# Kernel optimization log

Measured on AMD Instinct MI355X. Metric: run time of the kernel, lower is better.

The kernel has to match this reference:

```python
import jax, jax.numpy as jnp
import numpy as np

N_NODES = 50000


def _segment_mean(vals, seg_ids, num_segments):
    s = jax.ops.segment_sum(vals, seg_ids, num_segments=num_segments)
    cnt = jax.ops.segment_sum(jnp.ones((vals.shape[0],), vals.dtype), seg_ids,
                              num_segments=num_segments)
    return s / jnp.clip(cnt, 1.0)[:, None]


def _sage_layer(h, src, dst, W_self, W_neigh, b):
    # mean-aggregate neighbor messages: gather h[src], scatter-mean to dst
    neigh = _segment_mean(h[src], dst, N_NODES)
    return h @ W_self + neigh @ W_neigh + b


def _edge_score(h, src, dst, Wp, bp):
    # concat(h_u, h_v) @ Wp == h_u @ Wp[:d] + h_v @ Wp[d:]
    d = h.shape[1]
    return h[src] @ Wp[:d] + h[dst] @ Wp[d:] + bp


def setup_inputs() -> dict:
    key = jax.random.key(0)
    ks = jax.random.split(key, 16)
    N, E, EP, EN = N_NODES, 800000, 200000, 200000
    d_in, d_hid, d_out = 128, 256, 128
    inp = {
        'x': jax.random.normal(ks[0], (N, d_in), jnp.float32),
        'msg_src': jax.random.randint(ks[1], (E,), 0, N, jnp.int32),
        'msg_dst': jax.random.randint(ks[2], (E,), 0, N, jnp.int32),
        'pos_src': jax.random.randint(ks[3], (EP,), 0, N, jnp.int32),
        'pos_dst': jax.random.randint(ks[4], (EP,), 0, N, jnp.int32),
        'neg_src': jax.random.randint(ks[5], (EN,), 0, N, jnp.int32),
        'neg_dst': jax.random.randint(ks[6], (EN,), 0, N, jnp.int32),
        'W1_self': jax.random.normal(ks[7], (d_in, d_hid), jnp.float32) * 0.05,
        'W1_neigh': jax.random.normal(ks[8], (d_in, d_hid), jnp.float32) * 0.05,
        'b1': jnp.zeros((d_hid,), jnp.float32),
        'W2_self': jax.random.normal(ks[9], (d_hid, d_out), jnp.float32) * 0.05,
        'W2_neigh': jax.random.normal(ks[10], (d_hid, d_out), jnp.float32) * 0.05,
        'b2': jnp.zeros((d_out,), jnp.float32),
        'Wp': jax.random.normal(ks[11], (2 * d_out, 1), jnp.float32) * 0.05,
        'bp': jnp.zeros((1,), jnp.float32),
    }
    return inp


def reference(x, msg_src, msg_dst, pos_src, pos_dst, neg_src, neg_dst,
              W1_self, W1_neigh, b1, W2_self, W2_neigh, b2, Wp, bp):
    h = _sage_layer(x, msg_src, msg_dst, W1_self, W1_neigh, b1)
    h = jax.nn.relu(h)
    h = _sage_layer(h, msg_src, msg_dst, W2_self, W2_neigh, b2)
    pos_score = _edge_score(h, pos_src, pos_dst, Wp, bp)
    neg_score = _edge_score(h, neg_src, neg_dst, Wp, bp)
    return pos_score, neg_score
```

## Files before the change

### kernel.cpp

```cpp
#include <hip/hip_runtime.h>


#define NN 50000
#define EM 800000
#define EPOS 200000
#define ENEG 200000
#define NB 196
#define RPB 4096
#define MTILES 3125
#define GEMM_GRID 512
#define XCONV_BLOCKS 6250

typedef __bf16 bf16;
typedef bf16 bf16x2 __attribute__((ext_vector_type(2)));
typedef bf16 bf16x4 __attribute__((ext_vector_type(4)));
typedef bf16 bf16x8 __attribute__((ext_vector_type(8)));
typedef float floatx4 __attribute__((ext_vector_type(4)));

#define I_CNT  0
#define I_ROW  50176
#define I_BSUM 100608
#define I_BOFF 100864
#define I_CCUR 101120
#define I_CSR  101376
#define B_CREG 3605504
#define B_XB   10005504
#define B_AGG1 22805504
#define B_H1   35605504
#define B_NV   61205504
#define B_WT1  62005504
#define B_WT2  62136576
#define B_P    62267648
#define B_Q    62468352

__global__ __launch_bounds__(256) void count_kernel(const int* __restrict__ dst,
                                                    int* __restrict__ cnt, int n) {
    int i = blockIdx.x * blockDim.x + threadIdx.x;
    if (i < n) atomicAdd(&cnt[dst[i]], 1);
}

__global__ __launch_bounds__(256) void scan1_kernel(const int* __restrict__ cnt,
                                                    int* __restrict__ bsum) {
    __shared__ int s[256];
    int t = threadIdx.x;
    int i = blockIdx.x * 256 + t;
    s[t] = (i < NN) ? cnt[i] : 0;
    __syncthreads();
    for (int o = 128; o > 0; o >>= 1) {
        if (t < o) s[t] += s[t + o];
        __syncthreads();
    }
    if (t == 0) bsum[blockIdx.x] = s[0];
}

__global__ __launch_bounds__(256) void scan2_kernel(const int* __restrict__ bsum,
                                                    int* __restrict__ boff) {
    __shared__ int s[256];
    int t = threadIdx.x;
    s[t] = (t < NB) ? bsum[t] : 0;
    __syncthreads();
    for (int o = 1; o < 256; o <<= 1) {
        int u = (t >= o) ? s[t - o] : 0;
        __syncthreads();
        s[t] += u;
        __syncthreads();
    }
    if (t < NB) boff[t] = (t == 0) ? 0 : s[t - 1];
}

__global__ __launch_bounds__(256) void scan3_kernel(const int* __restrict__ cnt,
                                                    const int* __restrict__ boff,
                                                    int* __restrict__ rowstart,
                                                    int* __restrict__ ccur) {
    __shared__ int s[256];
    int t = threadIdx.x;
    int i = blockIdx.x * 256 + t;
    int v = (i < NN) ? cnt[i] : 0;
    s[t] = v;
    __syncthreads();
    for (int o = 1; o < 256; o <<= 1) {
        int u = (t >= o) ? s[t - o] : 0;
        __syncthreads();
        s[t] += u;
        __syncthreads();
    }
    int excl = boff[blockIdx.x] + s[t] - v;
    if (i < NN) rowstart[i] = excl;
    if (i == NN - 1) rowstart[NN] = EM;
    if (t == 0) ccur[blockIdx.x] = boff[blockIdx.x];
}

__global__ __launch_bounds__(256) void bin_kernel(const int* __restrict__ src,
                                                  const int* __restrict__ dst,
                                                  int* __restrict__ ccur,
                                                  unsigned long long* __restrict__ creg) {
    __shared__ int hist[NB];
    __shared__ int cnt2[NB];
    __shared__ int goff[NB];
    __shared__ int base[256];
    __shared__ unsigned long long sorted[RPB];
    int t = threadIdx.x;
    int e0 = blockIdx.x * RPB;
    int nrec = EM - e0; if (nrec > RPB) nrec = RPB;

    for (int i = t; i < NB; i += 256) { hist[i] = 0; cnt2[i] = 0; }
    __syncthreads();

    int myb[RPB / 256];
    unsigned long long myrec[RPB / 256];
#pragma unroll
    for (int j = 0; j < RPB / 256; ++j) {
        int idx = j * 256 + t;
        if (idx < nrec) {
            int s = src[e0 + idx], d = dst[e0 + idx];
            myb[j] = d >> 8;
            myrec[j] = ((unsigned long long)(unsigned)d << 32) | (unsigned)s;
            atomicAdd(&hist[myb[j]], 1);
        } else myb[j] = -1;
    }
    __syncthreads();

    base[t] = (t < NB) ? hist[t] : 0;
    __syncthreads();
    for (int o = 1; o < 256; o <<= 1) {
        int u = (t >= o) ? base[t - o] : 0;
        __syncthreads();
        base[t] += u;
        __syncthreads();
    }

    if (t < NB && hist[t] > 0) goff[t] = atomicAdd(&ccur[t], hist[t]);
#pragma unroll
    for (int j = 0; j < RPB / 256; ++j) {
        if (myb[j] >= 0) {
            int rk = atomicAdd(&cnt2[myb[j]], 1);
            sorted[base[myb[j]] - hist[myb[j]] + rk] = myrec[j];
        }
    }
    __syncthreads();

#pragma unroll
    for (int j = 0; j < RPB / 256; ++j) {
        int idx = j * 256 + t;
        if (idx < nrec) {
            unsigned long long rec = sorted[idx];
            int b = (int)(rec >> 40);
            int exb = base[b] - hist[b];
            creg[(size_t)goff[b] + (idx - exb)] = rec;
        }
    }
}

__global__ __launch_bounds__(256) void binsort_kernel(
    const unsigned long long* __restrict__ creg,
    const int* __restrict__ rowstart, int* __restrict__ csr) {
    __shared__ int lcur[256];
    int t = threadIdx.x;
    int node0 = blockIdx.x * 256;
    int nodes = NN - node0; if (nodes > 256) nodes = 256;
    if (t < nodes) lcur[t] = rowstart[node0 + t];
    __syncthreads();
    int beg = rowstart[node0];
    int end = rowstart[node0 + nodes];
    for (int i = beg + t; i < end; i += 256) {
        unsigned long long rec = creg[i];
        int s = (int)(rec & 0xffffffffu);
        int d = (int)(rec >> 32);
        int pos = atomicAdd(&lcur[d - node0], 1);
        csr[pos] = s;
    }
}

__global__ __launch_bounds__(256) void conv_kernel(
    const float* __restrict__ x, bf16* __restrict__ xb,
    const float* __restrict__ W1s, const float* __restrict__ W1n,
    const float* __restrict__ W2n, const float* __restrict__ W2s,
    bf16* __restrict__ Wt1, bf16* __restrict__ Wt2) {
    if (blockIdx.x < XCONV_BLOCKS) {
        int i = blockIdx.x * 256 + threadIdx.x;
        float4 v = ((const float4*)x)[i];
        bf16x4 o;
        o[0] = (bf16)v.x; o[1] = (bf16)v.y; o[2] = (bf16)v.z; o[3] = (bf16)v.w;
        *(bf16x4*)(xb + (size_t)i * 4) = o;
    } else {
        int i = (blockIdx.x - XCONV_BLOCKS) * 256 + threadIdx.x;
        if (i >= 65536) return;
        int n = i >> 8, k = i & 255;
        float w1 = (k < 128) ? W1s[k * 256 + n] : W1n[(k - 128) * 256 + n];
        Wt1[i] = (bf16)w1;
        float w2 = (n < 128) ? W2n[k * 128 + n] : W2s[k * 128 + (n - 128)];
        Wt2[i] = (bf16)w2;
    }
}

__global__ __launch_bounds__(256) void gather1_kernel(const bf16* __restrict__ feat,
                                                      const int* __restrict__ rowstart,
                                                      const int* __restrict__ csr,
                                                      bf16* __restrict__ agg) {
    int node = (blockIdx.x * 256 + threadIdx.x) >> 6;
    if (node >= NN) return;
    int lane = threadIdx.x & 63;
    int q = lane >> 4, r = lane & 15;
    int c = r * 8;
    int beg = rowstart[node], end = rowstart[node + 1];
    float acc[8] = {0.f, 0.f, 0.f, 0.f, 0.f, 0.f, 0.f, 0.f};
    for (int i = beg + q; i < end; i += 4) {
        int s = csr[i];
        bf16x8 v = *(const bf16x8*)(feat + (size_t)s * 128 + c);
#pragma unroll
        for (int u = 0; u < 8; ++u) acc[u] += (float)v[u];
    }
#pragma unroll
    for (int m = 16; m <= 32; m <<= 1)
#pragma unroll
        for (int u = 0; u < 8; ++u) acc[u] += __shfl_xor(acc[u], m);
    if (q == 0) {
        int deg = end - beg;
        float inv = 1.0f / (float)(deg > 0 ? deg : 1);
        bf16x8 o;
#pragma unroll
        for (int u = 0; u < 8; ++u) o[u] = (bf16)(acc[u] * inv);
        *(bf16x8*)(agg + (size_t)node * 128 + c) = o;
    }
}

__global__ __launch_bounds__(256) void gemm1_kernel(
    const bf16* __restrict__ xb, const bf16* __restrict__ aggb,
    const bf16* __restrict__ Wt, const float* __restrict__ b1,
    bf16* __restrict__ h1b) {
    int w = threadIdx.x >> 6;
    int lane = threadIdx.x & 63;
    int r = lane & 15, quad = lane >> 4;
    int colbase = w * 64;

    bf16x8 bfr[4][8];
#pragma unroll
    for (int t = 0; t < 4; ++t)
#pragma unroll
        for (int kk = 0; kk < 8; ++kk)
            bfr[t][kk] = *(const bf16x8*)(Wt + (size_t)(colbase + t * 16 + r) * 256
                                          + kk * 32 + quad * 8);
    float bb[4];
#pragma unroll
    for (int t = 0; t < 4; ++t) bb[t] = b1[colbase + t * 16 + r];

    for (int tile = blockIdx.x; tile < MTILES; tile += GEMM_GRID) {
        int m0 = tile * 16;
        int row = m0 + r;
        bf16x8 a[8];
#pragma unroll
        for (int kk = 0; kk < 4; ++kk)
            a[kk] = *(const bf16x8*)(xb + (size_t)row * 128 + kk * 32 + quad * 8);
#pragma unroll
        for (int kk = 4; kk < 8; ++kk)
            a[kk] = *(const bf16x8*)(aggb + (size_t)row * 128 + (kk - 4) * 32 + quad * 8);
        floatx4 acc[4];
#pragma unroll
        for (int t = 0; t < 4; ++t) acc[t] = (floatx4){0.f, 0.f, 0.f, 0.f};
#pragma unroll
        for (int kk = 0; kk < 8; ++kk)
#pragma unroll
            for (int t = 0; t < 4; ++t)
                acc[t] = __builtin_amdgcn_mfma_f32_16x16x32_bf16(a[kk], bfr[t][kk],
                                                                 acc[t], 0, 0, 0);
        int mb = m0 + quad * 4;
#pragma unroll
        for (int t = 0; t < 4; ++t) {
            int col = colbase + t * 16 + r;
#pragma unroll
            for (int rr = 0; rr < 4; ++rr) {
                float v = acc[t][rr] + bb[t];
                v = v > 0.f ? v : 0.f;
                h1b[(size_t)(mb + rr) * 256 + col] = (bf16)v;
            }
        }
    }
}

__global__ __launch_bounds__(256) void gemm2_kernel(
    const bf16* __restrict__ h1b, const bf16* __restrict__ Wt,
    const float* __restrict__ b2, const float* __restrict__ wp,
    float4* __restrict__ nodev) {
    __shared__ float lp[4][16];
    __shared__ float lq[4][16];
    int w = threadIdx.x >> 6;
    int lane = threadIdx.x & 63;
    int r = lane & 15, quad = lane >> 4;
    int colbase = w * 64;

    bf16x8 bfr[4][8];
#pragma unroll
    for (int t = 0; t < 4; ++t)
#pragma unroll
        for (int kk = 0; kk < 8; ++kk)
            bfr[t][kk] = *(const bf16x8*)(Wt + (size_t)(colbase + t * 16 + r) * 256
                                          + kk * 32 + quad * 8);
    float bb[4], wA[4], wB[4];
#pragma unroll
    for (int t = 0; t < 4; ++t) {
        int col = colbase + t * 16 + r;
        if (w < 2) {
            bb[t] = 0.f;
            wA[t] = wp[col];
            wB[t] = wp[128 + col];
        } else {
            int c2 = col - 128;
            bb[t] = b2[c2];
            wA[t] = wp[c2];
            wB[t] = wp[128 + c2];
        }
    }

    for (int tile = blockIdx.x; tile < MTILES; tile += GEMM_GRID) {
        int m0 = tile * 16;
        int row = m0 + r;
        bf16x8 a[8];
#pragma unroll
        for (int kk = 0; kk < 8; ++kk)
            a[kk] = *(const bf16x8*)(h1b + (size_t)row * 256 + kk * 32 + quad * 8);
        floatx4 acc[4];
#pragma unroll
        for (int t = 0; t < 4; ++t) acc[t] = (floatx4){0.f, 0.f, 0.f, 0.f};
#pragma unroll
        for (int kk = 0; kk < 8; ++kk)
#pragma unroll
            for (int t = 0; t < 4; ++t)
                acc[t] = __builtin_amdgcn_mfma_f32_16x16x32_bf16(a[kk], bfr[t][kk],
                                                                 acc[t], 0, 0, 0);
        float pacc[4], qacc[4];
#pragma unroll
        for (int rr = 0; rr < 4; ++rr) {
            float pr = 0.f, qr = 0.f;
#pragma unroll
            for (int t = 0; t < 4; ++t) {
                float v = acc[t][rr] + bb[t];
                pr += v * wA[t];
                qr += v * wB[t];
            }
            pacc[rr] = pr;
            qacc[rr] = qr;
        }
#pragma unroll
        for (int m = 1; m <= 8; m <<= 1) {
#pragma unroll
            for (int rr = 0; rr < 4; ++rr) {
                pacc[rr] += __shfl_xor(pacc[rr], m);
                qacc[rr] += __shfl_xor(qacc[rr], m);
            }
        }
        if (r == 0) {
#pragma unroll
            for (int rr = 0; rr < 4; ++rr) {
                lp[w][quad * 4 + rr] = pacc[rr];
                lq[w][quad * 4 + rr] = qacc[rr];
            }
        }
        __syncthreads();
        if (threadIdx.x < 16) {
            int rw = threadIdx.x;
            float4 o;
            o.x = lp[0][rw] + lp[1][rw];
            o.y = lq[0][rw] + lq[1][rw];
            o.z = lp[2][rw] + lp[3][rw];
            o.w = lq[2][rw] + lq[3][rw];
            nodev[m0 + rw] = o;
        }
        __syncthreads();
    }
}

__global__ __launch_bounds__(256) void gather2_kernel(
    const float4* __restrict__ nodev, const int* __restrict__ rowstart,
    const int* __restrict__ csr, float* __restrict__ p, float* __restrict__ q) {
    int t = threadIdx.x;
    int node = blockIdx.x * 16 + (t >> 4);
    if (node >= NN) return;
    int l = t & 15;
    int beg = rowstart[node], end = rowstart[node + 1];
    float pz = 0.f, qz = 0.f;
    for (int i = beg + l; i < end; i += 16) {
        float4 v = nodev[csr[i]];
        pz += v.x;
        qz += v.y;
    }
#pragma unroll
    for (int m = 8; m >= 1; m >>= 1) {
        pz += __shfl_xor(pz, m);
        qz += __shfl_xor(qz, m);
    }
    if (l == 0) {
        int deg = end - beg;
        float inv = 1.0f / (float)(deg > 0 ? deg : 1);
        float4 me = nodev[node];
        p[node] = me.z + pz * inv;
        q[node] = me.w + qz * inv;
    }
}

__global__ __launch_bounds__(256) void score_kernel(
    const int* __restrict__ psrc, const int* __restrict__ pdst,
    const int* __restrict__ nsrc, const int* __restrict__ ndst,
    const float* __restrict__ p, const float* __restrict__ q,
    const float* __restrict__ bp, float* __restrict__ out) {
    int i = blockIdx.x * blockDim.x + threadIdx.x;
    float b = bp[0];
    if (i < EPOS) {
        out[i] = p[psrc[i]] + q[pdst[i]] + b;
    } else if (i < EPOS + ENEG) {
        int j = i - EPOS;
        out[i] = p[nsrc[j]] + q[ndst[j]] + b;
    }
}

extern "C" void kernel_launch(void* const* d_in, const int* in_sizes, int n_in,
                              void* d_out, int out_size, void* d_ws, size_t ws_size,
                              hipStream_t stream) {
    const float* x    = (const float*)d_in[0];
    const int*   msrc = (const int*)d_in[1];
    const int*   mdst = (const int*)d_in[2];
    const int*   psrc = (const int*)d_in[3];
    const int*   pdst = (const int*)d_in[4];
    const int*   nsrc = (const int*)d_in[5];
    const int*   ndst = (const int*)d_in[6];
    const float* W1s  = (const float*)d_in[7];
    const float* W1n  = (const float*)d_in[8];
    const float* b1   = (const float*)d_in[9];
    const float* W2s  = (const float*)d_in[10];
    const float* W2n  = (const float*)d_in[11];
    const float* b2   = (const float*)d_in[12];
    const float* wp   = (const float*)d_in[13];
    const float* bp   = (const float*)d_in[14];

    char* ws = (char*)d_ws;
    int*   cnt      = (int*)ws + I_CNT;
    int*   rowstart = (int*)ws + I_ROW;
    int*   bsum     = (int*)ws + I_BSUM;
    int*   boff     = (int*)ws + I_BOFF;
    int*   ccur     = (int*)ws + I_CCUR;
    int*   csr_src  = (int*)ws + I_CSR;
    unsigned long long* creg = (unsigned long long*)(ws + B_CREG);
    bf16*   xb    = (bf16*)(ws + B_XB);
    bf16*   agg1b = (bf16*)(ws + B_AGG1);
    bf16*   h1b   = (bf16*)(ws + B_H1);
    float4* nodev = (float4*)(ws + B_NV);
    bf16*   Wt1   = (bf16*)(ws + B_WT1);
    bf16*   Wt2   = (bf16*)(ws + B_WT2);
    float*  p     = (float*)(ws + B_P);
    float*  q     = (float*)(ws + B_Q);
    float*  out   = (float*)d_out;

    hipMemsetAsync(cnt, 0, 50176 * sizeof(int), stream);

    count_kernel<<<(EM + 255) / 256, 256, 0, stream>>>(mdst, cnt, EM);
    scan1_kernel<<<NB, 256, 0, stream>>>(cnt, bsum);
    scan2_kernel<<<1, 256, 0, stream>>>(bsum, boff);
    scan3_kernel<<<NB, 256, 0, stream>>>(cnt, boff, rowstart, ccur);
    bin_kernel<<<(EM + RPB - 1) / RPB, 256, 0, stream>>>(msrc, mdst, ccur, creg);
    binsort_kernel<<<NB, 256, 0, stream>>>(creg, rowstart, csr_src);

    conv_kernel<<<XCONV_BLOCKS + 256, 256, 0, stream>>>(x, xb, W1s, W1n, W2n, W2s,
                                                        Wt1, Wt2);

    gather1_kernel<<<(NN + 3) / 4, 256, 0, stream>>>(xb, rowstart, csr_src, agg1b);
    gemm1_kernel<<<GEMM_GRID, 256, 0, stream>>>(xb, agg1b, Wt1, b1, h1b);
    gemm2_kernel<<<GEMM_GRID, 256, 0, stream>>>(h1b, Wt2, b2, wp, nodev);
    gather2_kernel<<<(NN + 15) / 16, 256, 0, stream>>>(nodev, rowstart, csr_src, p, q);
    score_kernel<<<(EPOS + ENEG + 255) / 256, 256, 0, stream>>>(
        psrc, pdst, nsrc, ndst, p, q, bp, out);
}
```

Before: 263.7 us.

## Fuse CSR count into conversion kernel and fuse layer-1 gather into GEMM

Result: slower. 284.4 us (+7.9%).

```diff
diff --git a/kernel.cpp b/kernel.cpp
--- a/kernel.cpp
+++ b/kernel.cpp
@@ -7,227 +7,185 @@
 #define ENEG 200000
 #define NB 196
 #define RPB 4096
+#define CBLK 196
 #define MTILES 3125
 #define GEMM_GRID 512
 #define XCONV_BLOCKS 6250
 
 typedef __bf16 bf16;
-typedef bf16 bf16x2 __attribute__((ext_vector_type(2)));
 typedef bf16 bf16x4 __attribute__((ext_vector_type(4)));
 typedef bf16 bf16x8 __attribute__((ext_vector_type(8)));
 typedef float floatx4 __attribute__((ext_vector_type(4)));
-
-#define I_CNT  0
-#define I_ROW  50176
-#define I_BSUM 100608
-#define I_BOFF 100864
-#define I_CCUR 101120
-#define I_CSR  101376
-#define B_CREG 3605504
-#define B_XB   10005504
-#define B_AGG1 22805504
-#define B_H1   35605504
-#define B_NV   61205504
-#define B_WT1  62005504
-#define B_WT2  62136576
-#define B_P    62267648
-#define B_Q    62468352
-
-__global__ __launch_bounds__(256) void count_kernel(const int* __restrict__ dst,
-                                                    int* __restrict__ cnt, int n) {
-    int i = blockIdx.x * blockDim.x + threadIdx.x;
-    if (i < n) atomicAdd(&cnt[dst[i]], 1);
-}
-
-__global__ __launch_bounds__(256) void scan1_kernel(const int* __restrict__ cnt,
-                                                    int* __restrict__ bsum) {
-    __shared__ int s[256];
-    int t = threadIdx.x;
-    int i = blockIdx.x * 256 + t;
-    s[t] = (i < NN) ? cnt[i] : 0;
-    __syncthreads();
-    for (int o = 128; o > 0; o >>= 1) {
-        if (t < o) s[t] += s[t + o];
-        __syncthreads();
-    }
-    if (t == 0) bsum[blockIdx.x] = s[0];
-}
-
-__global__ __launch_bounds__(256) void scan2_kernel(const int* __restrict__ bsum,
-                                                    int* __restrict__ boff) {
-    __shared__ int s[256];
-    int t = threadIdx.x;
-    s[t] = (t < NB) ? bsum[t] : 0;
-    __syncthreads();
-    for (int o = 1; o < 256; o <<= 1) {
-        int u = (t >= o) ? s[t - o] : 0;
-        __syncthreads();
-        s[t] += u;
-        __syncthreads();
-    }
-    if (t < NB) boff[t] = (t == 0) ? 0 : s[t - 1];
-}
-
-__global__ __launch_bounds__(256) void scan3_kernel(const int* __restrict__ cnt,
-                                                    const int* __restrict__ boff,
-                                                    int* __restrict__ rowstart,
-                                                    int* __restrict__ ccur) {
-    __shared__ int s[256];
-    int t = threadIdx.x;
-    int i = blockIdx.x * 256 + t;
-    int v = (i < NN) ? cnt[i] : 0;
-    s[t] = v;
-    __syncthreads();
-    for (int o = 1; o < 256; o <<= 1) {
-        int u = (t >= o) ? s[t - o] : 0;
-        __syncthreads();
-        s[t] += u;
-        __syncthreads();
-    }
-    int excl = boff[blockIdx.x] + s[t] - v;
-    if (i < NN) rowstart[i] = excl;
-    if (i == NN - 1) rowstart[NN] = EM;
-    if (t == 0) ccur[blockIdx.x] = boff[blockIdx.x];
-}
-
-__global__ __launch_bounds__(256) void bin_kernel(const int* __restrict__ src,
-                                                  const int* __restrict__ dst,
-                                                  int* __restrict__ ccur,
-                                                  unsigned long long* __restrict__ creg) {
-    __shared__ int hist[NB];
-    __shared__ int cnt2[NB];
-    __shared__ int goff[NB];
-    __shared__ int base[256];
-    __shared__ unsigned long long sorted[RPB];
-    int t = threadIdx.x;
-    int e0 = blockIdx.x * RPB;
-    int nrec = EM - e0; if (nrec > RPB) nrec = RPB;
-
-    for (int i = t; i < NB; i += 256) { hist[i] = 0; cnt2[i] = 0; }
-    __syncthreads();
-
-    int myb[RPB / 256];
-    unsigned long long myrec[RPB / 256];
-#pragma unroll
-    for (int j = 0; j < RPB / 256; ++j) {
-        int idx = j * 256 + t;
-        if (idx < nrec) {
-            int s = src[e0 + idx], d = dst[e0 + idx];
-            myb[j] = d >> 8;
-            myrec[j] = ((unsigned long long)(unsigned)d << 32) | (unsigned)s;
-            atomicAdd(&hist[myb[j]], 1);
-        } else myb[j] = -1;
-    }
-    __syncthreads();
-
-    base[t] = (t < NB) ? hist[t] : 0;
-    __syncthreads();
-    for (int o = 1; o < 256; o <<= 1) {
-        int u = (t >= o) ? base[t - o] : 0;
-        __syncthreads();
-        base[t] += u;
-        __syncthreads();
-    }
-
-    if (t < NB && hist[t] > 0) goff[t] = atomicAdd(&ccur[t], hist[t]);
-#pragma unroll
-    for (int j = 0; j < RPB / 256; ++j) {
-        if (myb[j] >= 0) {
-            int rk = atomicAdd(&cnt2[myb[j]], 1);
-            sorted[base[myb[j]] - hist[myb[j]] + rk] = myrec[j];
-        }
-    }
-    __syncthreads();
-
-#pragma unroll
-    for (int j = 0; j < RPB / 256; ++j) {
-        int idx = j * 256 + t;
-        if (idx < nrec) {
-            unsigned long long rec = sorted[idx];
-            int b = (int)(rec >> 40);
-            int exb = base[b] - hist[b];
-            creg[(size_t)goff[b] + (idx - exb)] = rec;
-        }
-    }
-}
-
-__global__ __launch_bounds__(256) void binsort_kernel(
-    const unsigned long long* __restrict__ creg,
-    const int* __restrict__ rowstart, int* __restrict__ csr) {
-    __shared__ int lcur[256];
-    int t = threadIdx.x;
-    int node0 = blockIdx.x * 256;
-    int nodes = NN - node0; if (nodes > 256) nodes = 256;
-    if (t < nodes) lcur[t] = rowstart[node0 + t];
-    __syncthreads();
-    int beg = rowstart[node0];
-    int end = rowstart[node0 + nodes];
-    for (int i = beg + t; i < end; i += 256) {
-        unsigned long long rec = creg[i];
-        int s = (int)(rec & 0xffffffffu);
-        int d = (int)(rec >> 32);
-        int pos = atomicAdd(&lcur[d - node0], 1);
-        csr[pos] = s;
-    }
-}
-
-__global__ __launch_bounds__(256) void conv_kernel(
+typedef unsigned long long u64;
+
+#define I_CC   0
+#define I_BOFF 256
+#define I_CCUR 768
+#define I_ROW  1024
+#define I_CSR  51456
+#define B_CREG 3405824
+#define B_XB   9805824
+#define B_H1   22605824
+#define B_NV   48205824
+#define B_WT1  49005824
+#define B_WT2  49136896
+#define B_P    49267968
+#define B_Q    49468672
+
+__global__ __launch_bounds__(256) void convc_kernel(
     const float* __restrict__ x, bf16* __restrict__ xb,
     const float* __restrict__ W1s, const float* __restrict__ W1n,
     const float* __restrict__ W2n, const float* __restrict__ W2s,
-    bf16* __restrict__ Wt1, bf16* __restrict__ Wt2) {
+    bf16* __restrict__ Wt1, bf16* __restrict__ Wt2,
+    const int* __restrict__ mdst, int* __restrict__ cc) {
     if (blockIdx.x < XCONV_BLOCKS) {
         int i = blockIdx.x * 256 + threadIdx.x;
         float4 v = ((const float4*)x)[i];
         bf16x4 o;
         o[0] = (bf16)v.x; o[1] = (bf16)v.y; o[2] = (bf16)v.z; o[3] = (bf16)v.w;
         *(bf16x4*)(xb + (size_t)i * 4) = o;
-    } else {
+    } else if (blockIdx.x < XCONV_BLOCKS + 256) {
         int i = (blockIdx.x - XCONV_BLOCKS) * 256 + threadIdx.x;
-        if (i >= 65536) return;
         int n = i >> 8, k = i & 255;
         float w1 = (k < 128) ? W1s[k * 256 + n] : W1n[(k - 128) * 256 + n];
         Wt1[i] = (bf16)w1;
         float w2 = (n < 128) ? W2n[k * 128 + n] : W2s[k * 128 + (n - 128)];
         Wt2[i] = (bf16)w2;
-    }
-}
-
-__global__ __launch_bounds__(256) void gather1_kernel(const bf16* __restrict__ feat,
-                                                      const int* __restrict__ rowstart,
-                                                      const int* __restrict__ csr,
-                                                      bf16* __restrict__ agg) {
-    int node = (blockIdx.x * 256 + threadIdx.x) >> 6;
-    if (node >= NN) return;
-    int lane = threadIdx.x & 63;
-    int q = lane >> 4, r = lane & 15;
-    int c = r * 8;
-    int beg = rowstart[node], end = rowstart[node + 1];
-    float acc[8] = {0.f, 0.f, 0.f, 0.f, 0.f, 0.f, 0.f, 0.f};
-    for (int i = beg + q; i < end; i += 4) {
-        int s = csr[i];
-        bf16x8 v = *(const bf16x8*)(feat + (size_t)s * 128 + c);
-#pragma unroll
-        for (int u = 0; u < 8; ++u) acc[u] += (float)v[u];
-    }
-#pragma unroll
-    for (int m = 16; m <= 32; m <<= 1)
-#pragma unroll
-        for (int u = 0; u < 8; ++u) acc[u] += __shfl_xor(acc[u], m);
-    if (q == 0) {
-        int deg = end - beg;
-        float inv = 1.0f / (float)(deg > 0 ? deg : 1);
-        bf16x8 o;
-#pragma unroll
-        for (int u = 0; u < 8; ++u) o[u] = (bf16)(acc[u] * inv);
-        *(bf16x8*)(agg + (size_t)node * 128 + c) = o;
-    }
-}
-
-__global__ __launch_bounds__(256) void gemm1_kernel(
-    const bf16* __restrict__ xb, const bf16* __restrict__ aggb,
-    const bf16* __restrict__ Wt, const float* __restrict__ b1,
-    bf16* __restrict__ h1b) {
+    } else {
+        __shared__ int h[NB];
+        int t = threadIdx.x;
+        int cb = blockIdx.x - (XCONV_BLOCKS + 256);
+        for (int i = t; i < NB; i += 256) h[i] = 0;
+        __syncthreads();
+        int e0 = cb * RPB;
+        int nrec = EM - e0; if (nrec > RPB) nrec = RPB;
+        for (int j = t; j < nrec; j += 256) atomicAdd(&h[mdst[e0 + j] >> 8], 1);
+        __syncthreads();
+        if (t < NB && h[t] > 0) atomicAdd(&cc[t], h[t]);
+    }
+}
+
+__global__ __launch_bounds__(256) void cscan_kernel(const int* __restrict__ cc,
+                                                    int* __restrict__ boff,
+                                                    int* __restrict__ ccur) {
+    __shared__ int s[256];
+    int t = threadIdx.x;
+    s[t] = (t < NB) ? cc[t] : 0;
+    __syncthreads();
+    for (int o = 1; o < 256; o <<= 1) {
+        int u = (t >= o) ? s[t - o] : 0;
+        __syncthreads();
+        s[t] += u;
+        __syncthreads();
+    }
+    int excl = (t == 0) ? 0 : s[t - 1];
+    if (t < NB) { boff[t] = excl; ccur[t] = excl; }
+    if (t == 0) boff[NB] = EM;
+}
+
+__global__ __launch_bounds__(256) void bin_kernel(const int* __restrict__ src,
+                                                  const int* __restrict__ dst,
+                                                  int* __restrict__ ccur,
+                                                  u64* __restrict__ creg) {
+    __shared__ int hist[NB];
+    __shared__ int cnt2[NB];
+    __shared__ int goff[NB];
+    __shared__ int base[256];
+    __shared__ u64 sorted[RPB];
+    int t = threadIdx.x;
+    int e0 = blockIdx.x * RPB;
+    int nrec = EM - e0; if (nrec > RPB) nrec = RPB;
+
+    for (int i = t; i < NB; i += 256) { hist[i] = 0; cnt2[i] = 0; }
+    __syncthreads();
+
+    int myb[RPB / 256];
+    u64 myrec[RPB / 256];
+#pragma unroll
+    for (int j = 0; j < RPB / 256; ++j) {
+        int idx = j * 256 + t;
+        if (idx < nrec) {
+            int s = src[e0 + idx], d = dst[e0 + idx];
+            myb[j] = d >> 8;
+            myrec[j] = ((u64)(unsigned)d << 32) | (unsigned)s;
+            atomicAdd(&hist[myb[j]], 1);
+        } else myb[j] = -1;
+    }
+    __syncthreads();
+
+    base[t] = (t < NB) ? hist[t] : 0;
+    __syncthreads();
+    for (int o = 1; o < 256; o <<= 1) {
+        int u = (t >= o) ? base[t - o] : 0;
+        __syncthreads();
+        base[t] += u;
+        __syncthreads();
+    }
+
+    if (t < NB && hist[t] > 0) goff[t] = atomicAdd(&ccur[t], hist[t]);
+#pragma unroll
+    for (int j = 0; j < RPB / 256; ++j) {
+        if (myb[j] >= 0) {
+            int rk = atomicAdd(&cnt2[myb[j]], 1);
+            sorted[base[myb[j]] - hist[myb[j]] + rk] = myrec[j];
+        }
+    }
+    __syncthreads();
+
+#pragma unroll
+    for (int j = 0; j < RPB / 256; ++j) {
+        int idx = j * 256 + t;
+        if (idx < nrec) {
+            u64 rec = sorted[idx];
+            int b = (int)(rec >> 40);
+            int exb = base[b] - hist[b];
+            creg[(size_t)goff[b] + (idx - exb)] = rec;
+        }
+    }
+}
+
+__global__ __launch_bounds__(256) void binsort_kernel(
+    const u64* __restrict__ creg, const int* __restrict__ boff,
+    int* __restrict__ rowstart, int* __restrict__ csr) {
+    __shared__ int lcnt[256];
+    __shared__ int sc[256];
+    __shared__ int lcur[256];
+    int b = blockIdx.x, t = threadIdx.x;
+    int beg = boff[b], end = boff[b + 1];
+    lcnt[t] = 0;
+    __syncthreads();
+    for (int i = beg + t; i < end; i += 256) {
+        int d = (int)(creg[i] >> 32);
+        atomicAdd(&lcnt[d & 255], 1);
+    }
+    __syncthreads();
+    sc[t] = lcnt[t];
+    __syncthreads();
+    for (int o = 1; o < 256; o <<= 1) {
+        int u = (t >= o) ? sc[t - o] : 0;
+        __syncthreads();
+        sc[t] += u;
+        __syncthreads();
+    }
+    int excl = beg + sc[t] - lcnt[t];
+    int node = b * 256 + t;
+    if (node < NN) rowstart[node] = excl;
+    if (b == NB - 1 && t == 0) rowstart[NN] = EM;
+    lcur[t] = excl;
+    __syncthreads();
+    for (int i = beg + t; i < end; i += 256) {
+        u64 rec = creg[i];
+        int d = (int)(rec >> 32);
+        int pos = atomicAdd(&lcur[d & 255], 1);
+        csr[pos] = (int)(rec & 0xffffffffu);
+    }
+}
+
+__global__ __launch_bounds__(256) void ggemm1_kernel(
+    const bf16* __restrict__ xb, const int* __restrict__ rowstart,
+    const int* __restrict__ csr, const bf16* __restrict__ Wt,
+    const float* __restrict__ b1, bf16* __restrict__ h1b) {
+    __shared__ bf16 sAgg[16][136];
     int w = threadIdx.x >> 6;
     int lane = threadIdx.x & 63;
     int r = lane & 15, quad = lane >> 4;
@@ -246,6 +204,33 @@
 
     for (int tile = blockIdx.x; tile < MTILES; tile += GEMM_GRID) {
         int m0 = tile * 16;
+#pragma unroll
+        for (int jj = 0; jj < 4; ++jj) {
+            int idx = jj * 4 + w;
+            int node = m0 + idx;
+            int beg = rowstart[node], end = rowstart[node + 1];
+            int c = r * 8;
+            float acc[8] = {0.f, 0.f, 0.f, 0.f, 0.f, 0.f, 0.f, 0.f};
+            for (int i = beg + quad; i < end; i += 4) {
+                int s = csr[i];
+                bf16x8 v = *(const bf16x8*)(xb + (size_t)s * 128 + c);
+#pragma unroll
+                for (int u = 0; u < 8; ++u) acc[u] += (float)v[u];
+            }
+#pragma unroll
+            for (int m = 16; m <= 32; m <<= 1)
+#pragma unroll
+                for (int u = 0; u < 8; ++u) acc[u] += __shfl_xor(acc[u], m);
+            if (quad == 0) {
+                int deg = end - beg;
+                float inv = 1.0f / (float)(deg > 0 ? deg : 1);
+                bf16x8 o;
+#pragma unroll
+                for (int u = 0; u < 8; ++u) o[u] = (bf16)(acc[u] * inv);
+                *(bf16x8*)(&sAgg[idx][c]) = o;
+            }
+        }
+        __syncthreads();
         int row = m0 + r;
         bf16x8 a[8];
 #pragma unroll
@@ -253,27 +238,28 @@
             a[kk] = *(const bf16x8*)(xb + (size_t)row * 128 + kk * 32 + quad * 8);
 #pragma unroll
         for (int kk = 4; kk < 8; ++kk)
-            a[kk] = *(const bf16x8*)(aggb + (size_t)row * 128 + (kk - 4) * 32 + quad * 8);
-        floatx4 acc[4];
-#pragma unroll
-        for (int t = 0; t < 4; ++t) acc[t] = (floatx4){0.f, 0.f, 0.f, 0.f};
+            a[kk] = *(const bf16x8*)(&sAgg[r][(kk - 4) * 32 + quad * 8]);
+        floatx4 acc4[4];
+#pragma unroll
+        for (int t = 0; t < 4; ++t) acc4[t] = (floatx4){0.f, 0.f, 0.f, 0.f};
 #pragma unroll
         for (int kk = 0; kk < 8; ++kk)
 #pragma unroll
             for (int t = 0; t < 4; ++t)
-                acc[t] = __builtin_amdgcn_mfma_f32_16x16x32_bf16(a[kk], bfr[t][kk],
-                                                                 acc[t], 0, 0, 0);
+                acc4[t] = __builtin_amdgcn_mfma_f32_16x16x32_bf16(a[kk], bfr[t][kk],
+                                                                  acc4[t], 0, 0, 0);
         int mb = m0 + quad * 4;
 #pragma unroll
         for (int t = 0; t < 4; ++t) {
             int col = colbase + t * 16 + r;
 #pragma unroll
             for (int rr = 0; rr < 4; ++rr) {
-                float v = acc[t][rr] + bb[t];
+                float v = acc4[t][rr] + bb[t];
                 v = v > 0.f ? v : 0.f;
                 h1b[(size_t)(mb + rr) * 256 + col] = (bf16)v;
             }
         }
+        __syncthreads();
     }
 }
 
@@ -432,37 +418,30 @@
     const float* bp   = (const float*)d_in[14];
 
     char* ws = (char*)d_ws;
-    int*   cnt      = (int*)ws + I_CNT;
-    int*   rowstart = (int*)ws + I_ROW;
-    int*   bsum     = (int*)ws + I_BSUM;
+    int*   cc       = (int*)ws + I_CC;
     int*   boff     = (int*)ws + I_BOFF;
     int*   ccur     = (int*)ws + I_CCUR;
+    int*   rowstart = (int*)ws + I_ROW;
     int*   csr_src  = (int*)ws + I_CSR;
-    unsigned long long* creg = (unsigned long long*)(ws + B_CREG);
-    bf16*   xb    = (bf16*)(ws + B_XB);
-    bf16*   agg1b = (bf16*)(ws + B_AGG1);
-    bf16*   h1b   = (bf16*)(ws + B_H1);
+    u64*   creg  = (u64*)(ws + B_CREG);
+    bf16*  xb    = (bf16*)(ws + B_XB);
+    bf16*  h1b   = (bf16*)(ws + B_H1);
     float4* nodev = (float4*)(ws + B_NV);
-    bf16*   Wt1   = (bf16*)(ws + B_WT1);
-    bf16*   Wt2   = (bf16*)(ws + B_WT2);
-    float*  p     = (float*)(ws + B_P);
-    float*  q     = (float*)(ws + B_Q);
-    float*  out   = (float*)d_out;
-
-    hipMemsetAsync(cnt, 0, 50176 * sizeof(int), stream);
-
-    count_kernel<<<(EM + 255) / 256, 256, 0, stream>>>(mdst, cnt, EM);
-    scan1_kernel<<<NB, 256, 0, stream>>>(cnt, bsum);
-    scan2_kernel<<<1, 256, 0, stream>>>(bsum, boff);
-    scan3_kernel<<<NB, 256, 0, stream>>>(cnt, boff, rowstart, ccur);
+    bf16*  Wt1   = (bf16*)(ws + B_WT1);
+    bf16*  Wt2   = (bf16*)(ws + B_WT2);
+    float* p     = (float*)(ws + B_P);
+    float* q     = (float*)(ws + B_Q);
+    float* out   = (float*)d_out;
+
+    hipMemsetAsync(cc, 0, 256 * sizeof(int), stream);
+
+    convc_kernel<<<XCONV_BLOCKS + 256 + CBLK, 256, 0, stream>>>(
+        x, xb, W1s, W1n, W2n, W2s, Wt1, Wt2, mdst, cc);
+    cscan_kernel<<<1, 256, 0, stream>>>(cc, boff, ccur);
     bin_kernel<<<(EM + RPB - 1) / RPB, 256, 0, stream>>>(msrc, mdst, ccur, creg);
-    binsort_kernel<<<NB, 256, 0, stream>>>(creg, rowstart, csr_src);
-
-    conv_kernel<<<XCONV_BLOCKS + 256, 256, 0, stream>>>(x, xb, W1s, W1n, W2n, W2s,
-                                                        Wt1, Wt2);
-
-    gather1_kernel<<<(NN + 3) / 4, 256, 0, stream>>>(xb, rowstart, csr_src, agg1b);
-    gemm1_kernel<<<GEMM_GRID, 256, 0, stream>>>(xb, agg1b, Wt1, b1, h1b);
+    binsort_kernel<<<NB, 256, 0, stream>>>(creg, boff, rowstart, csr_src);
+
+    ggemm1_kernel<<<GEMM_GRID, 256, 0, stream>>>(xb, rowstart, csr_src, Wt1, b1, h1b);
     gemm2_kernel<<<GEMM_GRID, 256, 0, stream>>>(h1b, Wt2, b2, wp, nodev);
     gather2_kernel<<<(NN + 15) / 16, 256, 0, stream>>>(nodev, rowstart, csr_src, p, q);
     score_kernel<<<(EPOS + ENEG + 255) / 256, 256, 0, stream>>>(
```
